# Optimization experiments

Measured on AMD Instinct MI355X. Metric: run time of the kernel, lower is better.

Reference implementation:

```python
import jax, jax.numpy as jnp
import numpy as np

NOISE_EPS = 1e-2   # Shazeer noisy-gating stddev floor
LN_EPS = 1e-6
LOSS_COEF = 0.01
K = 2              # num_activated_experts


def _layer_norm(x, w, b):
    mu = jnp.mean(x, axis=-1, keepdims=True)
    var = jnp.var(x, axis=-1, keepdims=True)
    return (x - mu) * jax.lax.rsqrt(var + LN_EPS) * w + b


def _cv_squared(v):
    return jnp.var(v) / (jnp.mean(v) ** 2 + 1e-10)


def _normal_cdf(z):
    return 0.5 * (1.0 + jax.scipy.special.erf(z / jnp.sqrt(jnp.asarray(2.0, z.dtype))))


def setup_inputs() -> dict:
    key = jax.random.key(0)
    ks = jax.random.split(key, 8)
    N, D, H, O, E = 8192, 512, 1024, 512, 8
    x = jax.random.normal(ks[0], (N, D), jnp.float32)
    x_offsets = jnp.sort(jax.random.randint(ks[1], (17,), 0, N)).astype(jnp.int64)
    noise = jax.random.normal(ks[2], (N, E), jnp.float32)
    s = 0.02
    return {
        "x": x,
        "x_offsets": x_offsets,
        "max_seq_len": 2048,
        "noise": noise,
        "norm_w": jnp.ones((D,), jnp.float32),
        "norm_bias": jnp.zeros((D,), jnp.float32),
        "w_gate": jax.random.normal(ks[3], (D, E), jnp.float32) * s,
        "w_noise": jax.random.normal(ks[4], (D, E), jnp.float32) * s,
        "W1": jax.random.normal(ks[5], (E, H, D), jnp.float32) * s,  # [E, model_d, input]
        "b1": jnp.zeros((E, H), jnp.float32),
        "W2": jax.random.normal(ks[6], (E, O, H), jnp.float32) * s,  # [E, output, model_d]
        "b2": jnp.zeros((E, O), jnp.float32),
        "output_weight": jax.random.normal(ks[7], (D, O), jnp.float32) * s,
    }


def reference(x, x_offsets, max_seq_len, noise, norm_w, norm_bias, w_gate, w_noise,
              W1, b1, W2, b2, output_weight):
    N, D = x.shape
    E = w_gate.shape[1]
    k_plus = min(K + 1, E)

    # pre-norm
    x_norm = _layer_norm(x, norm_w, norm_bias)

    # noisy top-k gating (training path)
    clean_logits = x_norm @ w_gate                      # [N, E]
    noise_stddev = jax.nn.softplus(x_norm @ w_noise) + NOISE_EPS
    noisy_logits = clean_logits + noise * noise_stddev

    top_logits, top_indices = jax.lax.top_k(noisy_logits, k_plus)   # [N, k+1]
    top_k_logits = top_logits[:, :K]
    top_k_indices = top_indices[:, :K]
    top_k_gates = jax.nn.softmax(top_k_logits, axis=-1)             # [N, K]

    rows = jnp.arange(N)[:, None]
    gates = jnp.zeros((N, E), top_k_gates.dtype).at[rows, top_k_indices].set(top_k_gates)

    # load = prob each expert is in top-k under the gating noise (Shazeer)
    flat = top_logits.reshape(-1)
    pos_in = jnp.arange(N) * k_plus + K
    thr_in = flat[pos_in][:, None]          # (k+1)-th value: threshold if already in
    thr_out = flat[pos_in - 1][:, None]     # k-th value: threshold if currently out
    is_in = noisy_logits > thr_in
    prob_in = _normal_cdf((clean_logits - thr_in) / noise_stddev)
    prob_out = _normal_cdf((clean_logits - thr_out) / noise_stddev)
    load_probs = jnp.where(is_in, prob_in, prob_out)                # [N, E]

    loss = LOSS_COEF * (_cv_squared(gates.sum(0)) + _cv_squared(load_probs.sum(0)))

    # dispatch stats: tokens per expert
    lengths = jnp.zeros((E,), jnp.float32).at[top_k_indices.reshape(-1)].add(1.0)
    load = lengths / lengths.sum()

    # grouped expert MLP (dense one-hot combine; gates are 0 for unrouted experts)
    h = jnp.einsum('nd,ehd->neh', x_norm, W1) + b1                  # [N, E, H]
    a = jax.nn.silu(h)
    y_e = jnp.einsum('neh,eoh->neo', a, W2) + b2                    # [N, E, O]
    y_moe = jnp.einsum('ne,neo->no', gates, y_e)                    # [N, O]

    # shared expert: addmm(y, shared_x=x, output_weight)
    y = y_moe + x @ output_weight
    return y, loss, load
```

## Files before the change

### kernel.cpp

```cpp
#include <hip/hip_runtime.h>
#include <math.h>

typedef unsigned short u16;
typedef unsigned int u32;

#define N_ROWS 8192
#define DDIM 512
#define HDIM 1024
#define ODIM 512
#define NEXP 8
#define MAXPAIRS (N_ROWS * 2)
#define MAXPOS (MAXPAIRS + NEXP * 128)
#define MAXTILES (MAXPOS / 128)

#define SM_CNT 0
#define SM_CUR 8
#define SM_AOFF 16
#define SM_GSUM 32
#define SM_LSUM 40
#define SM_WORDS 64

using short8 = __attribute__((ext_vector_type(8))) short;
using float4v = __attribute__((ext_vector_type(4))) float;

__device__ __forceinline__ u16 f2bf(float f) {
    union { float f; u32 u; } v; v.f = f;
    u32 u = v.u;
    return (u16)((u + 0x7fffu + ((u >> 16) & 1u)) >> 16);
}

__device__ __forceinline__ void async_copy16(u16* lds, const u16* g) {
    __builtin_amdgcn_global_load_lds(
        (const __attribute__((address_space(1))) void*)g,
        (__attribute__((address_space(3))) void*)lds, 16, 0, 0);
}

#define CONV_BLOCKS 8192
__global__ __launch_bounds__(256) void prep_kernel(
    const float* __restrict__ W1, const float* __restrict__ W2, const float* __restrict__ ow,
    u16* __restrict__ W1b, u16* __restrict__ W2b, u16* __restrict__ owT,
    int* __restrict__ small, int* __restrict__ bucket_rows, float* __restrict__ zeropage)
{
    __shared__ float tile[32][33];
    int b = blockIdx.x, tid = threadIdx.x;
    if (b < CONV_BLOCKS) {
        const size_t n4 = (size_t)NEXP * HDIM * DDIM / 4;
        size_t i = (size_t)b * 256 + tid;
        const float* src; u16* dst;
        if (i < n4) { src = W1; dst = W1b; } else { src = W2; dst = W2b; i -= n4; }
        float4 v = ((const float4*)src)[i];
        ushort4 o;
        o.x = f2bf(v.x); o.y = f2bf(v.y); o.z = f2bf(v.z); o.w = f2bf(v.w);
        ((ushort4*)dst)[i] = o;
    } else if (b < CONV_BLOCKS + 256) {
        int t = b - CONV_BLOCKS;
        int bx = (t & 15) * 32, by = (t >> 4) * 32;
        int tx = tid & 31, ty = tid >> 5;
        for (int r = ty; r < 32; r += 8) tile[r][tx] = ow[(size_t)(by + r) * ODIM + bx + tx];
        __syncthreads();
        for (int r = ty; r < 32; r += 8) owT[(size_t)(bx + r) * DDIM + by + tx] = f2bf(tile[tx][r]);
    } else {
        int i = (b - CONV_BLOCKS - 256) * 256 + tid;
        if (i < SM_WORDS) small[i] = 0;
        if (i < 512) zeropage[i] = 0.f;
        if (i < MAXPOS) bucket_rows[i] = -1;
    }
}

__global__ __launch_bounds__(256) void gating_kernel(
    const float* __restrict__ x, const float* __restrict__ noise,
    const float* __restrict__ norm_w, const float* __restrict__ norm_b,
    const float* __restrict__ w_gate, const float* __restrict__ w_noise,
    u16* __restrict__ xnorm_bf, u16* __restrict__ x_bf,
    int* __restrict__ pair_expert, float* __restrict__ pair_gate,
    int* __restrict__ small)
{
    __shared__ float wgT[NEXP * DDIM];
    __shared__ float wnT[NEXP * DDIM];
    __shared__ float blk_g[NEXP];
    __shared__ float blk_l[NEXP];
    __shared__ int blk_c[NEXP];
    float* smf = (float*)small;

    int tid = threadIdx.x;
    for (int i = tid; i < NEXP * DDIM; i += 256) {
        int d = i >> 3, e = i & 7;
        wgT[e * DDIM + d] = w_gate[i];
        wnT[e * DDIM + d] = w_noise[i];
    }
    if (tid < NEXP) { blk_g[tid] = 0.f; blk_l[tid] = 0.f; blk_c[tid] = 0; }
    __syncthreads();

    int wave = tid >> 6, lane = tid & 63;
    float nw[8], nb[8];
#pragma unroll
    for (int j = 0; j < 8; j++) { nw[j] = norm_w[j * 64 + lane]; nb[j] = norm_b[j * 64 + lane]; }

    for (int r = 0; r < 4; ++r) {
        int row = blockIdx.x * 16 + wave * 4 + r;
        const float* xr = x + (size_t)row * DDIM;
        float xv[8], s = 0.f, s2 = 0.f;
#pragma unroll
        for (int j = 0; j < 8; j++) { float v = xr[j * 64 + lane]; xv[j] = v; s += v; s2 += v * v; }
#pragma unroll
        for (int o = 32; o; o >>= 1) { s += __shfl_xor(s, o, 64); s2 += __shfl_xor(s2, o, 64); }
        float mu = s * (1.f / DDIM);
        float var = s2 * (1.f / DDIM) - mu * mu;
        float rstd = rsqrtf(var + 1e-6f);

        float acc[16];
#pragma unroll
        for (int e = 0; e < 16; e++) acc[e] = 0.f;
#pragma unroll
        for (int j = 0; j < 8; j++) {
            float v = (xv[j] - mu) * rstd * nw[j] + nb[j];
            int d = j * 64 + lane;
            xnorm_bf[(size_t)row * DDIM + d] = f2bf(v);
            x_bf[(size_t)row * DDIM + d] = f2bf(xv[j]);
#pragma unroll
            for (int e = 0; e < 8; e++) {
                acc[e] += v * wgT[e * DDIM + d];
                acc[8 + e] += v * wnT[e * DDIM + d];
            }
        }
#pragma unroll
        for (int e = 0; e < 16; e++)
#pragma unroll
            for (int o = 32; o; o >>= 1) acc[e] += __shfl_xor(acc[e], o, 64);

        float cl[8], sd[8], nz[8];
#pragma unroll
        for (int e = 0; e < 8; e++) {
            cl[e] = acc[e];
            float t = acc[8 + e];
            float sp = fmaxf(t, 0.f) + log1pf(expf(-fabsf(t)));
            sd[e] = sp + 0.01f;
            nz[e] = cl[e] + noise[(size_t)row * NEXP + e] * sd[e];
        }
        int idx[3]; float val[3]; u32 msk = 0;
#pragma unroll
        for (int t = 0; t < 3; t++) {
            float best = -INFINITY; int bi = 0;
#pragma unroll
            for (int e = 0; e < 8; e++)
                if (!((msk >> e) & 1) && nz[e] > best) { best = nz[e]; bi = e; }
            idx[t] = bi; val[t] = best; msk |= 1u << bi;
        }
        float e1 = expf(val[1] - val[0]);
        float g0 = 1.f / (1.f + e1), g1 = e1 / (1.f + e1);
        float thr_in = val[2], thr_out = val[1];

        if (lane == 0) {
            pair_expert[row * 2] = idx[0]; pair_gate[row * 2] = g0;
            pair_expert[row * 2 + 1] = idx[1]; pair_gate[row * 2 + 1] = g1;
            atomicAdd(&blk_g[idx[0]], g0); atomicAdd(&blk_g[idx[1]], g1);
            atomicAdd(&blk_c[idx[0]], 1); atomicAdd(&blk_c[idx[1]], 1);
#pragma unroll
            for (int e = 0; e < 8; e++) {
                float thr = (nz[e] > thr_in) ? thr_in : thr_out;
                float z = (cl[e] - thr) / sd[e];
                float p = 0.5f * (1.f + erff(z * 0.70710678118654752f));
                atomicAdd(&blk_l[e], p);
            }
        }
    }
    __syncthreads();
    if (tid < NEXP) {
        atomicAdd(smf + SM_GSUM + tid, blk_g[tid]);
        atomicAdd(smf + SM_LSUM + tid, blk_l[tid]);
        atomicAdd(&small[SM_CNT + tid], blk_c[tid]);
    }
}

__global__ __launch_bounds__(256) void scatter_kernel(
    const int* __restrict__ pair_expert, const float* __restrict__ pair_gate,
    int* __restrict__ small, int* __restrict__ bucket_rows, float* __restrict__ gate_by_pos,
    float* __restrict__ out_loss, float* __restrict__ out_load)
{
    __shared__ int aoff[NEXP + 1];
    __shared__ int blk_cnt[NEXP];
    __shared__ int blk_base[NEXP];
    int tid = threadIdx.x;
    if (tid == 0) {
        int acc = 0; aoff[0] = 0;
        for (int e = 0; e < NEXP; e++) { acc += (small[SM_CNT + e] + 127) & ~127; aoff[e + 1] = acc; }
    }
    if (tid < NEXP) blk_cnt[tid] = 0;
    __syncthreads();
    int p = blockIdx.x * 256 + tid;
    int e = pair_expert[p];
    int local = atomicAdd(&blk_cnt[e], 1);
    __syncthreads();
    if (tid < NEXP)
        blk_base[tid] = aoff[tid] + atomicAdd(&small[SM_CUR + tid], blk_cnt[tid]);
    if (blockIdx.x == 0 && tid < NEXP + 1) small[SM_AOFF + tid] = aoff[tid];
    __syncthreads();
    int pos = blk_base[e] + local;
    bucket_rows[pos] = p >> 1;
    gate_by_pos[pos] = pair_gate[p];

    if (blockIdx.x == 0 && tid == 0) {
        const float* gs = (const float*)small + SM_GSUM;
        const float* ls = (const float*)small + SM_LSUM;
        float cv[2];
        for (int t = 0; t < 2; t++) {
            const float* v = t ? ls : gs;
            float m = 0.f;
            for (int k = 0; k < NEXP; k++) m += v[k];
            m *= (1.f / NEXP);
            float var = 0.f;
            for (int k = 0; k < NEXP; k++) { float d = v[k] - m; var += d * d; }
            var *= (1.f / NEXP);
            cv[t] = var / (m * m + 1e-10f);
        }
        out_loss[0] = 0.01f * (cv[0] + cv[1]);
        int tot = 0;
        for (int k = 0; k < NEXP; k++) tot += small[SM_CNT + k];
        float inv = 1.f / (float)tot;
        for (int k = 0; k < NEXP; k++) out_load[k] = (float)small[SM_CNT + k] * inv;
    }
}


__global__ __launch_bounds__(256) void gemmA_kernel(
    const u16* __restrict__ xnorm, const u16* __restrict__ xbf,
    const u16* __restrict__ W1b, const u16* __restrict__ owT,
    const int* __restrict__ bucket_rows, const int* __restrict__ small,
    const float* __restrict__ b1, const u16* __restrict__ zeropage,
    u16* __restrict__ a_buf, float* __restrict__ y)
{
    constexpr int KD = 512;
    __shared__ __align__(16) u16 As[128 * 64];
    __shared__ __align__(16) u16 Bs[64 * 64];

    int tid = threadIdx.x;
    bool m0 = blockIdx.y < 16;
    int base, bn, e = 0;
    const u16* Bsel;
    if (m0) {
        base = blockIdx.x * 128;
        if (base >= small[SM_AOFF + 8]) return;
        while (e < 7 && base >= small[SM_AOFF + e + 1]) ++e;
        bn = blockIdx.y * 64;
        Bsel = W1b + (size_t)e * HDIM * KD;
    } else {
        int j = (blockIdx.y - 16) * 136 + blockIdx.x;
        if (j >= 512) return;
        base = (j >> 3) * 128;
        bn = (j & 7) * 64;
        Bsel = owT;
    }

    int wave = tid >> 6, lane = tid & 63;
    int lr = lane >> 3;
    int lc = ((lane & 7) ^ lr) * 8;

    const u16* ga[4]; const u16* gb[2];
    u16* la[4]; u16* lb[2];
#pragma unroll
    for (int c = 0; c < 4; c++) {
        int tr = wave * 32 + c * 8;
        if (m0) {
            int r0 = bucket_rows[base + tr + lr];
            ga[c] = ((r0 < 0) ? zeropage : xnorm + (size_t)r0 * KD) + lc;
        } else {
            ga[c] = xbf + (size_t)(base + tr + lr) * KD + lc;
        }
        la[c] = &As[tr * 64];
    }
#pragma unroll
    for (int c = 0; c < 2; c++) {
        int tr = wave * 16 + c * 8;
        gb[c] = Bsel + (size_t)(bn + tr + lr) * KD + lc;
        lb[c] = &Bs[tr * 64];
    }

    int wm = (wave & 1) * 64, wn = (wave >> 1) * 32;
    int fr = lane & 15, kq = lane >> 4, f7 = fr & 7;

    float4v acc[4][2];
#pragma unroll
    for (int i = 0; i < 4; i++)
#pragma unroll
        for (int j = 0; j < 2; j++) acc[i][j] = (float4v){0.f, 0.f, 0.f, 0.f};

    for (int k0 = 0; k0 < KD; k0 += 64) {
        __syncthreads();
#pragma unroll
        for (int c = 0; c < 4; c++) async_copy16(la[c], ga[c] + k0);
#pragma unroll
        for (int c = 0; c < 2; c++) async_copy16(lb[c], gb[c] + k0);
        __syncthreads();
        short8 af[4][2], bf[2][2];
#pragma unroll
        for (int mt = 0; mt < 4; mt++)
#pragma unroll
            for (int kh = 0; kh < 2; kh++)
                af[mt][kh] = *(const short8*)&As[(wm + mt * 16 + fr) * 64 + (((kq + 4 * kh) ^ f7) * 8)];
#pragma unroll
        for (int nt = 0; nt < 2; nt++)
#pragma unroll
            for (int kh = 0; kh < 2; kh++)
                bf[nt][kh] = *(const short8*)&Bs[(wn + nt * 16 + fr) * 64 + (((kq + 4 * kh) ^ f7) * 8)];
#pragma unroll
        for (int mt = 0; mt < 4; mt++)
#pragma unroll
            for (int nt = 0; nt < 2; nt++) {
                acc[mt][nt] = __builtin_amdgcn_mfma_f32_16x16x32_bf16(af[mt][0], bf[nt][0], acc[mt][nt], 0, 0, 0);
                acc[mt][nt] = __builtin_amdgcn_mfma_f32_16x16x32_bf16(af[mt][1], bf[nt][1], acc[mt][nt], 0, 0, 0);
            }
    }

    int rbase = (lane >> 4) * 4, c16 = lane & 15;
#pragma unroll
    for (int nt = 0; nt < 2; nt++) {
        int gn = bn + wn + nt * 16 + c16;
        float bv = m0 ? b1[e * HDIM + gn] : 0.f;
#pragma unroll
        for (int mt = 0; mt < 4; mt++) {
            int gm = base + wm + mt * 16 + rbase;
#pragma unroll
            for (int r = 0; r < 4; r++) {
                float v = acc[mt][nt][r];
                if (m0) {
                    float h = v + bv;
                    float a = h * __builtin_amdgcn_rcpf(1.f + __expf(-h));
                    a_buf[(size_t)(gm + r) * HDIM + gn] = f2bf(a);
                } else {
                    y[(size_t)(gm + r) * ODIM + gn] = v;
                }
            }
        }
    }
}

__global__ __launch_bounds__(256) void gemmB_kernel(
    const u16* __restrict__ a_buf, const u16* __restrict__ W2b,
    const int* __restrict__ bucket_rows, const int* __restrict__ small,
    const float* __restrict__ b2, const float* __restrict__ gate_by_pos,
    float* __restrict__ y)
{
    constexpr int KD = 1024;
    constexpr int KS = 512;
    __shared__ __align__(16) u16 As[128 * 64];
    __shared__ __align__(16) u16 Bs[64 * 64];

    int tid = threadIdx.x;
    int base = blockIdx.x * 128;
    if (base >= small[SM_AOFF + 8]) return;
    int e = 0;
    while (e < 7 && base >= small[SM_AOFF + e + 1]) ++e;
    int bn = (blockIdx.y >> 1) * 64;
    int koff = (blockIdx.y & 1) * KS;

    int wave = tid >> 6, lane = tid & 63;
    int lr = lane >> 3;
    int lc = ((lane & 7) ^ lr) * 8;

    const u16* Bsel = W2b + (size_t)e * ODIM * KD;
    const u16* ga[4]; const u16* gb[2];
    u16* la[4]; u16* lb[2];
#pragma unroll
    for (int c = 0; c < 4; c++) {
        int tr = wave * 32 + c * 8;
        ga[c] = a_buf + (size_t)(base + tr + lr) * KD + koff + lc;
        la[c] = &As[tr * 64];
    }
#pragma unroll
    for (int c = 0; c < 2; c++) {
        int tr = wave * 16 + c * 8;
        gb[c] = Bsel + (size_t)(bn + tr + lr) * KD + koff + lc;
        lb[c] = &Bs[tr * 64];
    }

    int wm = (wave & 1) * 64, wn = (wave >> 1) * 32;
    int fr = lane & 15, kq = lane >> 4, f7 = fr & 7;

    float4v acc[4][2];
#pragma unroll
    for (int i = 0; i < 4; i++)
#pragma unroll
        for (int j = 0; j < 2; j++) acc[i][j] = (float4v){0.f, 0.f, 0.f, 0.f};

    for (int k0 = 0; k0 < KS; k0 += 64) {
        __syncthreads();
#pragma unroll
        for (int c = 0; c < 4; c++) async_copy16(la[c], ga[c] + k0);
#pragma unroll
        for (int c = 0; c < 2; c++) async_copy16(lb[c], gb[c] + k0);
        __syncthreads();
        short8 af[4][2], bf[2][2];
#pragma unroll
        for (int mt = 0; mt < 4; mt++)
#pragma unroll
            for (int kh = 0; kh < 2; kh++)
                af[mt][kh] = *(const short8*)&As[(wm + mt * 16 + fr) * 64 + (((kq + 4 * kh) ^ f7) * 8)];
#pragma unroll
        for (int nt = 0; nt < 2; nt++)
#pragma unroll
            for (int kh = 0; kh < 2; kh++)
                bf[nt][kh] = *(const short8*)&Bs[(wn + nt * 16 + fr) * 64 + (((kq + 4 * kh) ^ f7) * 8)];
#pragma unroll
        for (int mt = 0; mt < 4; mt++)
#pragma unroll
            for (int nt = 0; nt < 2; nt++) {
                acc[mt][nt] = __builtin_amdgcn_mfma_f32_16x16x32_bf16(af[mt][0], bf[nt][0], acc[mt][nt], 0, 0, 0);
                acc[mt][nt] = __builtin_amdgcn_mfma_f32_16x16x32_bf16(af[mt][1], bf[nt][1], acc[mt][nt], 0, 0, 0);
            }
    }

    float bscale = (blockIdx.y & 1) ? 0.f : 1.f;
    int rbase = (lane >> 4) * 4, c16 = lane & 15;
#pragma unroll
    for (int mt = 0; mt < 4; mt++) {
        int pos0 = base + wm + mt * 16 + rbase;
        int rows[4]; float gs[4];
#pragma unroll
        for (int r = 0; r < 4; r++) { rows[r] = bucket_rows[pos0 + r]; gs[r] = gate_by_pos[pos0 + r]; }
#pragma unroll
        for (int nt = 0; nt < 2; nt++) {
            int gn = bn + wn + nt * 16 + c16;
            float b2v = b2[e * ODIM + gn] * bscale;
#pragma unroll
            for (int r = 0; r < 4; r++) {
                if (rows[r] >= 0)
                    unsafeAtomicAdd(&y[(size_t)rows[r] * ODIM + gn], gs[r] * (acc[mt][nt][r] + b2v));
            }
        }
    }
}

extern "C" void kernel_launch(void* const* d_in, const int* in_sizes, int n_in,
                              void* d_out, int out_size, void* d_ws, size_t ws_size,
                              hipStream_t stream)
{
    (void)in_sizes; (void)n_in; (void)out_size; (void)ws_size;
    const float* x = (const float*)d_in[0];
    const float* noise = (const float*)d_in[3];
    const float* norm_w = (const float*)d_in[4];
    const float* norm_b = (const float*)d_in[5];
    const float* w_gate = (const float*)d_in[6];
    const float* w_noise = (const float*)d_in[7];
    const float* W1 = (const float*)d_in[8];
    const float* b1 = (const float*)d_in[9];
    const float* W2 = (const float*)d_in[10];
    const float* b2 = (const float*)d_in[11];
    const float* ow = (const float*)d_in[12];

    float* y = (float*)d_out;
    float* out_loss = y + (size_t)N_ROWS * ODIM;
    float* out_load = out_loss + 1;

    char* ws = (char*)d_ws;
    size_t off = 0;
    auto alloc = [&](size_t b) { size_t p = off; off = (off + b + 255) & ~(size_t)255; return p; };
    u16* xnorm_bf = (u16*)(ws + alloc((size_t)N_ROWS * DDIM * 2));
    u16* x_bf     = (u16*)(ws + alloc((size_t)N_ROWS * DDIM * 2));
    u16* W1b      = (u16*)(ws + alloc((size_t)NEXP * HDIM * DDIM * 2));
    u16* W2b      = (u16*)(ws + alloc((size_t)NEXP * ODIM * HDIM * 2));
    u16* owT      = (u16*)(ws + alloc((size_t)DDIM * ODIM * 2));
    u16* a_buf    = (u16*)(ws + alloc((size_t)MAXPOS * HDIM * 2));
    int* pair_expert = (int*)(ws + alloc((size_t)MAXPAIRS * 4));
    float* pair_gate = (float*)(ws + alloc((size_t)MAXPAIRS * 4));
    float* gate_by_pos = (float*)(ws + alloc((size_t)MAXPOS * 4));
    int* bucket_rows = (int*)(ws + alloc((size_t)MAXPOS * 4));
    int* small       = (int*)(ws + alloc(SM_WORDS * 4));
    float* zeropage  = (float*)(ws + alloc(2048));

    prep_kernel<<<CONV_BLOCKS + 256 + 68, 256, 0, stream>>>(W1, W2, ow, W1b, W2b, owT,
                                                            small, bucket_rows, zeropage);
    gating_kernel<<<N_ROWS / 16, 256, 0, stream>>>(x, noise, norm_w, norm_b, w_gate, w_noise,
                                                   xnorm_bf, x_bf, pair_expert, pair_gate, small);
    scatter_kernel<<<MAXPAIRS / 256, 256, 0, stream>>>(pair_expert, pair_gate, small,
                                                       bucket_rows, gate_by_pos, out_loss, out_load);
    gemmA_kernel<<<dim3(MAXTILES, 16 + 4), 256, 0, stream>>>(xnorm_bf, x_bf, W1b, owT, bucket_rows,
                                                             small, b1, (const u16*)zeropage, a_buf, y);
    gemmB_kernel<<<dim3(MAXTILES, 16), 256, 0, stream>>>(a_buf, W2b, bucket_rows, small,
                                                         b2, gate_by_pos, y);
}
```

Baseline: 277.6 us.

## Double-buffer LDS tiles in expert GEMMs and drop split-K in second GEMM

Both grouped GEMM kernels now use two LDS buffers: the next K-slice is prefetched with async copies while MFMAs run on the current one, leaving one barrier per iteration instead of two. The second GEMM also stops splitting K across two blocks. Each block now covers the full hidden dimension, which halves the atomic adds into the output and removes the bias-scaling trick. The cost is double the shared memory per block and half as many blocks for the second GEMM, each with a longer K loop.

```diff
diff --git a/kernel.cpp b/kernel.cpp
--- a/kernel.cpp
+++ b/kernel.cpp
@@ -230,8 +230,9 @@
     u16* __restrict__ a_buf, float* __restrict__ y)
 {
     constexpr int KD = 512;
-    __shared__ __align__(16) u16 As[128 * 64];
-    __shared__ __align__(16) u16 Bs[64 * 64];
+    constexpr int NIT = KD / 64;
+    __shared__ __align__(16) u16 As[2][128 * 64];
+    __shared__ __align__(16) u16 Bs[2][64 * 64];
 
     int tid = threadIdx.x;
     bool m0 = blockIdx.y < 16;
@@ -256,7 +257,7 @@
     int lc = ((lane & 7) ^ lr) * 8;
 
     const u16* ga[4]; const u16* gb[2];
-    u16* la[4]; u16* lb[2];
+    int lao[4], lbo[2];
 #pragma unroll
     for (int c = 0; c < 4; c++) {
         int tr = wave * 32 + c * 8;
@@ -266,13 +267,13 @@
         } else {
             ga[c] = xbf + (size_t)(base + tr + lr) * KD + lc;
         }
-        la[c] = &As[tr * 64];
+        lao[c] = tr * 64;
     }
 #pragma unroll
     for (int c = 0; c < 2; c++) {
         int tr = wave * 16 + c * 8;
         gb[c] = Bsel + (size_t)(bn + tr + lr) * KD + lc;
-        lb[c] = &Bs[tr * 64];
+        lbo[c] = tr * 64;
     }
 
     int wm = (wave & 1) * 64, wn = (wave >> 1) * 32;
@@ -284,24 +285,32 @@
 #pragma unroll
         for (int j = 0; j < 2; j++) acc[i][j] = (float4v){0.f, 0.f, 0.f, 0.f};
 
-    for (int k0 = 0; k0 < KD; k0 += 64) {
+#pragma unroll
+    for (int c = 0; c < 4; c++) async_copy16(&As[0][lao[c]], ga[c]);
+#pragma unroll
+    for (int c = 0; c < 2; c++) async_copy16(&Bs[0][lbo[c]], gb[c]);
+
+    for (int k = 0; k < NIT; ++k) {
+        int cur = k & 1, nxt = cur ^ 1;
         __syncthreads();
-#pragma unroll
-        for (int c = 0; c < 4; c++) async_copy16(la[c], ga[c] + k0);
-#pragma unroll
-        for (int c = 0; c < 2; c++) async_copy16(lb[c], gb[c] + k0);
-        __syncthreads();
+        if (k + 1 < NIT) {
+            int off = (k + 1) * 64;
+#pragma unroll
+            for (int c = 0; c < 4; c++) async_copy16(&As[nxt][lao[c]], ga[c] + off);
+#pragma unroll
+            for (int c = 0; c < 2; c++) async_copy16(&Bs[nxt][lbo[c]], gb[c] + off);
+        }
         short8 af[4][2], bf[2][2];
 #pragma unroll
         for (int mt = 0; mt < 4; mt++)
 #pragma unroll
             for (int kh = 0; kh < 2; kh++)
-                af[mt][kh] = *(const short8*)&As[(wm + mt * 16 + fr) * 64 + (((kq + 4 * kh) ^ f7) * 8)];
+                af[mt][kh] = *(const short8*)&As[cur][(wm + mt * 16 + fr) * 64 + (((kq + 4 * kh) ^ f7) * 8)];
 #pragma unroll
         for (int nt = 0; nt < 2; nt++)
 #pragma unroll
             for (int kh = 0; kh < 2; kh++)
-                bf[nt][kh] = *(const short8*)&Bs[(wn + nt * 16 + fr) * 64 + (((kq + 4 * kh) ^ f7) * 8)];
+                bf[nt][kh] = *(const short8*)&Bs[cur][(wn + nt * 16 + fr) * 64 + (((kq + 4 * kh) ^ f7) * 8)];
 #pragma unroll
         for (int mt = 0; mt < 4; mt++)
 #pragma unroll
@@ -341,17 +350,16 @@
     float* __restrict__ y)
 {
     constexpr int KD = 1024;
-    constexpr int KS = 512;
-    __shared__ __align__(16) u16 As[128 * 64];
-    __shared__ __align__(16) u16 Bs[64 * 64];
+    constexpr int NIT = KD / 64;
+    __shared__ __align__(16) u16 As[2][128 * 64];
+    __shared__ __align__(16) u16 Bs[2][64 * 64];
 
     int tid = threadIdx.x;
     int base = blockIdx.x * 128;
     if (base >= small[SM_AOFF + 8]) return;
     int e = 0;
     while (e < 7 && base >= small[SM_AOFF + e + 1]) ++e;
-    int bn = (blockIdx.y >> 1) * 64;
-    int koff = (blockIdx.y & 1) * KS;
+    int bn = blockIdx.y * 64;
 
     int wave = tid >> 6, lane = tid & 63;
     int lr = lane >> 3;
@@ -359,18 +367,18 @@
 
     const u16* Bsel = W2b + (size_t)e * ODIM * KD;
     const u16* ga[4]; const u16* gb[2];
-    u16* la[4]; u16* lb[2];
+    int lao[4], lbo[2];
 #pragma unroll
     for (int c = 0; c < 4; c++) {
         int tr = wave * 32 + c * 8;
-        ga[c] = a_buf + (size_t)(base + tr + lr) * KD + koff + lc;
-        la[c] = &As[tr * 64];
+        ga[c] = a_buf + (size_t)(base + tr + lr) * KD + lc;
+        lao[c] = tr * 64;
     }
 #pragma unroll
     for (int c = 0; c < 2; c++) {
         int tr = wave * 16 + c * 8;
-        gb[c] = Bsel + (size_t)(bn + tr + lr) * KD + koff + lc;
-        lb[c] = &Bs[tr * 64];
+        gb[c] = Bsel + (size_t)(bn + tr + lr) * KD + lc;
+        lbo[c] = tr * 64;
     }
 
     int wm = (wave & 1) * 64, wn = (wave >> 1) * 32;
@@ -382,24 +390,32 @@
 #pragma unroll
         for (int j = 0; j < 2; j++) acc[i][j] = (float4v){0.f, 0.f, 0.f, 0.f};
 
-    for (int k0 = 0; k0 < KS; k0 += 64) {
+#pragma unroll
+    for (int c = 0; c < 4; c++) async_copy16(&As[0][lao[c]], ga[c]);
+#pragma unroll
+    for (int c = 0; c < 2; c++) async_copy16(&Bs[0][lbo[c]], gb[c]);
+
+    for (int k = 0; k < NIT; ++k) {
+        int cur = k & 1, nxt = cur ^ 1;
         __syncthreads();
-#pragma unroll
-        for (int c = 0; c < 4; c++) async_copy16(la[c], ga[c] + k0);
-#pragma unroll
-        for (int c = 0; c < 2; c++) async_copy16(lb[c], gb[c] + k0);
-        __syncthreads();
+        if (k + 1 < NIT) {
+            int off = (k + 1) * 64;
+#pragma unroll
+            for (int c = 0; c < 4; c++) async_copy16(&As[nxt][lao[c]], ga[c] + off);
+#pragma unroll
+            for (int c = 0; c < 2; c++) async_copy16(&Bs[nxt][lbo[c]], gb[c] + off);
+        }
         short8 af[4][2], bf[2][2];
 #pragma unroll
         for (int mt = 0; mt < 4; mt++)
 #pragma unroll
             for (int kh = 0; kh < 2; kh++)
-                af[mt][kh] = *(const short8*)&As[(wm + mt * 16 + fr) * 64 + (((kq + 4 * kh) ^ f7) * 8)];
+                af[mt][kh] = *(const short8*)&As[cur][(wm + mt * 16 + fr) * 64 + (((kq + 4 * kh) ^ f7) * 8)];
 #pragma unroll
         for (int nt = 0; nt < 2; nt++)
 #pragma unroll
             for (int kh = 0; kh < 2; kh++)
-                bf[nt][kh] = *(const short8*)&Bs[(wn + nt * 16 + fr) * 64 + (((kq + 4 * kh) ^ f7) * 8)];
+                bf[nt][kh] = *(const short8*)&Bs[cur][(wn + nt * 16 + fr) * 64 + (((kq + 4 * kh) ^ f7) * 8)];
 #pragma unroll
         for (int mt = 0; mt < 4; mt++)
 #pragma unroll
@@ -409,7 +425,6 @@
             }
     }
 
-    float bscale = (blockIdx.y & 1) ? 0.f : 1.f;
     int rbase = (lane >> 4) * 4, c16 = lane & 15;
 #pragma unroll
     for (int mt = 0; mt < 4; mt++) {
@@ -420,7 +435,7 @@
 #pragma unroll
         for (int nt = 0; nt < 2; nt++) {
             int gn = bn + wn + nt * 16 + c16;
-            float b2v = b2[e * ODIM + gn] * bscale;
+            float b2v = b2[e * ODIM + gn];
 #pragma unroll
             for (int r = 0; r < 4; r++) {
                 if (rows[r] >= 0)
@@ -475,6 +490,6 @@
                                                        bucket_rows, gate_by_pos, out_loss, out_load);
     gemmA_kernel<<<dim3(MAXTILES, 16 + 4), 256, 0, stream>>>(xnorm_bf, x_bf, W1b, owT, bucket_rows,
                                                              small, b1, (const u16*)zeropage, a_buf, y);
-    gemmB_kernel<<<dim3(MAXTILES, 16), 256, 0, stream>>>(a_buf, W2b, bucket_rows, small,
-                                                         b2, gate_by_pos, y);
-}
+    gemmB_kernel<<<dim3(MAXTILES, ODIM / 64), 256, 0, stream>>>(a_buf, W2b, bucket_rows, small,
+                                                                b2, gate_by_pos, y);
+}
```

Result: no change. 276.9 us (-0.3%).
